# Performance work log

Measured on AMD Instinct MI355X. Metric: run time of the kernel, lower is better.

## Reference

```python
import jax, jax.numpy as jnp
import numpy as np

B, L, D, H, V = 4, 2048, 512, 8, 50257
NCAND, K, MAXM, NL, DFF = 64, 5, 10, 2, 4 * 512
HD = D // H


def _ln(x, g, b, eps=1e-5):
    m = jnp.mean(x, -1, keepdims=True)
    v = jnp.mean((x - m) ** 2, -1, keepdims=True)
    return (x - m) * jax.lax.rsqrt(v + eps) * g + b


def _mha(x, in_w, in_b, out_w, out_b):
    Bx, Lx, Dx = x.shape
    qkv = x @ in_w.T + in_b                      # [B,L,3D]
    q, k, v = jnp.split(qkv, 3, axis=-1)
    heads = lambda t: t.reshape(Bx, Lx, H, HD).transpose(0, 2, 1, 3)  # [B,H,L,hd]
    q, k, v = heads(q), heads(k), heads(v)
    s = jnp.einsum('bhqd,bhkd->bhqk', q, k) * np.float32(1.0 / np.sqrt(HD))
    a = jax.nn.softmax(s, axis=-1)
    o = jnp.einsum('bhqk,bhkd->bhqd', a, v).transpose(0, 2, 1, 3).reshape(Bx, Lx, Dx)
    return o @ out_w.T + out_b


def _encoder(x, p):
    # torch TransformerEncoderLayer default: post-LN, ReLU, dropout off (eval)
    for i in range(NL):
        x = _ln(x + _mha(x, p['attn_in_w'][i], p['attn_in_b'][i], p['attn_out_w'][i], p['attn_out_b'][i]), p['ln1_g'][i], p['ln1_b'][i])
        h = jax.nn.relu(x @ p['ffn_w1'][i].T + p['ffn_b1'][i]) @ p['ffn_w2'][i].T + p['ffn_b2'][i]
        x = _ln(x + h, p['ln2_g'][i], p['ln2_b'][i])
    return x


def _forward(token_ids, candidate_embeds, p):
    x = p['tok_emb'][token_ids] + p['pos_emb'][jnp.arange(L)][None]
    hidden = _encoder(x, p)                                  # [B,L,D]
    start_logits = hidden @ p['start_w'] + p['start_b']      # [B,L]
    end_logits = hidden @ p['end_w'] + p['end_b']
    s_idx = jax.lax.top_k(start_logits, K)[1]                # [B,K]
    e_idx = jax.lax.top_k(end_logits, K)[1]
    valid = (e_idx >= s_idx) & ((e_idx - s_idx) < MAXM)      # span validity mask
    h_s = jnp.take_along_axis(hidden, s_idx[..., None], axis=1)  # [B,K,D]
    h_e = jnp.take_along_axis(hidden, e_idx[..., None], axis=1)
    feat = jnp.concatenate([h_s, h_e, h_s * h_e], axis=-1)   # [B,K,3D]
    span = jax.nn.relu(feat @ p['span_w1'].T + p['span_b1']) @ p['span_w2'].T + p['span_b2']
    # compact valid spans to the front (ragged-to-padded), pad rest with zeros
    order = jnp.argsort((~valid).astype(jnp.int32), axis=1)  # stable: valid first
    span = jnp.take_along_axis(span, order[..., None], axis=1)
    vs = jnp.take_along_axis(valid, order, axis=1)
    span = span * vs[..., None].astype(span.dtype)           # [B,K,D]
    mp = span @ p['mention_w'].T + p['mention_b']
    cp = candidate_embeds @ p['entity_w'].T + p['entity_b']
    scores = jnp.einsum('bmd,bmcd->bmc', mp, cp)             # [B,K,NCAND]
    return span, start_logits, end_logits, hidden, scores


PARAM_KEYS = ['tok_emb', 'pos_emb', 'attn_in_w', 'attn_in_b', 'attn_out_w', 'attn_out_b',
              'ln1_g', 'ln1_b', 'ffn_w1', 'ffn_b1', 'ffn_w2', 'ffn_b2', 'ln2_g', 'ln2_b',
              'start_w', 'start_b', 'end_w', 'end_b', 'span_w1', 'span_b1', 'span_w2', 'span_b2',
              'mention_w', 'mention_b', 'entity_w', 'entity_b']


def setup_inputs() -> dict:
    key = jax.random.key(0)
    ks = iter(jax.random.split(key, 32))
    n = lambda shape, s=0.02: jax.random.normal(next(ks), shape, jnp.float32) * s
    return {
        'token_ids': jax.random.randint(next(ks), (B, L), 0, V),
        'candidate_embeds': jax.random.normal(next(ks), (B, K, NCAND, D), jnp.float32),
        'tok_emb': n((V, D)), 'pos_emb': n((L, D)),
        'attn_in_w': n((NL, 3 * D, D)), 'attn_in_b': n((NL, 3 * D)),
        'attn_out_w': n((NL, D, D)), 'attn_out_b': n((NL, D)),
        'ln1_g': jnp.ones((NL, D)), 'ln1_b': jnp.zeros((NL, D)),
        'ffn_w1': n((NL, DFF, D)), 'ffn_b1': n((NL, DFF)),
        'ffn_w2': n((NL, D, DFF)), 'ffn_b2': n((NL, D)),
        'ln2_g': jnp.ones((NL, D)), 'ln2_b': jnp.zeros((NL, D)),
        'start_w': n((D,)), 'start_b': jnp.zeros(()),
        'end_w': n((D,)), 'end_b': jnp.zeros(()),
        'span_w1': n((D, 3 * D)), 'span_b1': jnp.zeros((D,)),
        'span_w2': n((D, D)), 'span_b2': jnp.zeros((D,)),
        'mention_w': n((D, D)), 'mention_b': jnp.zeros((D,)),
        'entity_w': n((D, D)), 'entity_b': jnp.zeros((D,)),
    }


def reference(token_ids, candidate_embeds, tok_emb, pos_emb, attn_in_w, attn_in_b, attn_out_w, attn_out_b,
              ln1_g, ln1_b, ffn_w1, ffn_b1, ffn_w2, ffn_b2, ln2_g, ln2_b,
              start_w, start_b, end_w, end_b, span_w1, span_b1, span_w2, span_b2,
              mention_w, mention_b, entity_w, entity_b):
    loc = locals()
    p = {k: loc[k] for k in PARAM_KEYS}
    return _forward(token_ids, candidate_embeds, p)
```

## Files before the change

### kernel.cpp

```cpp
#include <hip/hip_runtime.h>
#include <hip/hip_bf16.h>
#include <cstddef>

#define BQ 4
#define LQ 2048
#define DQ 512
#define HQ 8
#define HDQ 64
#define KQ 5
#define MAXMQ 10

typedef __attribute__((ext_vector_type(8))) __bf16 bf16x8;
typedef __attribute__((ext_vector_type(4))) float f32x4;

__device__ inline void gload_lds16(const void* g, void* l) {
  __builtin_amdgcn_global_load_lds(
      (const __attribute__((address_space(1))) unsigned*)g,
      (__attribute__((address_space(3))) unsigned*)l, 16, 0, 0);
}

__device__ inline unsigned pack_bf16(float a, float b) {
  unsigned short ua = __builtin_bit_cast(unsigned short, (__bf16)a);
  unsigned short ub = __builtin_bit_cast(unsigned short, (__bf16)b);
  return (unsigned)ua | ((unsigned)ub << 16);
}

__device__ inline unsigned pack2(__bf16 a, __bf16 b) {
  return (unsigned)__builtin_bit_cast(unsigned short, a) |
         ((unsigned)__builtin_bit_cast(unsigned short, b) << 16);
}

__global__ __launch_bounds__(256) void cvt4_kernel(
    const float* __restrict__ s0, const float* __restrict__ s1,
    const float* __restrict__ s2, const float* __restrict__ s3,
    __bf16* __restrict__ d0, __bf16* __restrict__ d1,
    __bf16* __restrict__ d2, __bf16* __restrict__ d3) {
  size_t g = ((size_t)blockIdx.x * 256 + threadIdx.x) * 8;
  const float* src; __bf16* dst; size_t e;
  if (g < 1572864)      { src = s0; dst = d0; e = g; }
  else if (g < 2097152) { src = s1; dst = d1; e = g - 1572864; }
  else if (g < 4194304) { src = s2; dst = d2; e = g - 2097152; }
  else                  { src = s3; dst = d3; e = g - 4194304; }
  float4 a = *(const float4*)(src + e);
  float4 b = *(const float4*)(src + e + 4);
  bf16x8 t;
  t[0] = (__bf16)a.x; t[1] = (__bf16)a.y; t[2] = (__bf16)a.z; t[3] = (__bf16)a.w;
  t[4] = (__bf16)b.x; t[5] = (__bf16)b.y; t[6] = (__bf16)b.z; t[7] = (__bf16)b.w;
  *(bf16x8*)(dst + e) = t;
}

__global__ __launch_bounds__(256) void transpose512_kernel(const float* __restrict__ in,
                                                           float* __restrict__ out) {
  __shared__ float t[32][33];
  int bx = blockIdx.x & 15, by = blockIdx.x >> 4;
  int cx = threadIdx.x & 31, ry = threadIdx.x >> 5;
  #pragma unroll
  for (int i = 0; i < 4; ++i)
    t[ry + i * 8][cx] = in[(size_t)(by * 32 + ry + i * 8) * 512 + bx * 32 + cx];
  __syncthreads();
  #pragma unroll
  for (int i = 0; i < 4; ++i)
    out[(size_t)(bx * 32 + ry + i * 8) * 512 + by * 32 + cx] = t[cx][ry + i * 8];
}

__global__ __launch_bounds__(256) void embed_kernel(const int* __restrict__ tok,
    const float* __restrict__ te, const float* __restrict__ pe,
    float* __restrict__ x, __bf16* __restrict__ xb) {
  int row = blockIdx.x;
  int l = row & (LQ - 1);
  int t = tok[row];
  const float* trow = te + (size_t)t * DQ;
  const float* prow = pe + (size_t)l * DQ;
  float* xr = x + (size_t)row * DQ;
  __bf16* xbr = xb + (size_t)row * DQ;
  for (int d = threadIdx.x; d < DQ; d += 256) {
    float v = trow[d] + prow[d];
    xr[d] = v;
    xbr[d] = (__bf16)v;
  }
}

template<int BN, bool RELU, bool HASRES, bool WF32, bool WBF16>
__global__ __launch_bounds__(256) void bgemm_kernel(
    const __bf16* __restrict__ A, const __bf16* __restrict__ W,
    const float* __restrict__ bias, const float* __restrict__ R,
    float* __restrict__ C, __bf16* __restrict__ Cb, int M, int N, int K) {
  __shared__ __bf16 As[2][128][32];
  __shared__ __bf16 Bs[2][BN][32];
  constexpr int NF = BN / 32;
  const int tid = threadIdx.x;
  const int w = tid >> 6, lane = tid & 63;
  const int lr = lane & 15, lg = lane >> 4;
  const int wr = w >> 1, wc = w & 1;
  const int m0 = blockIdx.y * 128, n0 = blockIdx.x * BN;

  f32x4 acc[4][NF];
  #pragma unroll
  for (int m = 0; m < 4; ++m)
    #pragma unroll
    for (int n = 0; n < NF; ++n) acc[m][n] = f32x4{0.f, 0.f, 0.f, 0.f};

  const int srowA = w * 32 + (lane >> 2);
  const int scol = (lane & 3) * 8;
  const int srowB = (BN == 128) ? srowA : (w * 16 + (lane >> 2));
  const __bf16* Ag = A + (size_t)(m0 + srowA) * K + scol;
  const __bf16* Bg = W + (size_t)(n0 + srowB) * K + scol;

  gload_lds16(Ag, &As[0][w * 32][0]);
  gload_lds16(Ag + 16 * K, &As[0][w * 32 + 16][0]);
  if (BN == 128) {
    gload_lds16(Bg, &Bs[0][(w * 32) % BN][0]);
    gload_lds16(Bg + 16 * K, &Bs[0][(w * 32 + 16) % BN][0]);
  } else {
    gload_lds16(Bg, &Bs[0][(w * 16) % BN][0]);
  }

  const int NT = K / 32;
  for (int t = 0; t < NT; ++t) {
    const int cur = t & 1;
    __syncthreads();
    if (t + 1 < NT) {
      const int k1 = (t + 1) * 32;
      gload_lds16(Ag + k1, &As[cur ^ 1][w * 32][0]);
      gload_lds16(Ag + 16 * K + k1, &As[cur ^ 1][w * 32 + 16][0]);
      if (BN == 128) {
        gload_lds16(Bg + k1, &Bs[cur ^ 1][(w * 32) % BN][0]);
        gload_lds16(Bg + 16 * K + k1, &Bs[cur ^ 1][(w * 32 + 16) % BN][0]);
      } else {
        gload_lds16(Bg + k1, &Bs[cur ^ 1][(w * 16) % BN][0]);
      }
    }
    bf16x8 af[4], bfr[NF];
    #pragma unroll
    for (int m = 0; m < 4; ++m) af[m] = *(bf16x8*)&As[cur][wr * 64 + m * 16 + lr][lg * 8];
    #pragma unroll
    for (int n = 0; n < NF; ++n) bfr[n] = *(bf16x8*)&Bs[cur][wc * (BN / 2) + n * 16 + lr][lg * 8];
    #pragma unroll
    for (int m = 0; m < 4; ++m)
      #pragma unroll
      for (int n = 0; n < NF; ++n)
        acc[m][n] = __builtin_amdgcn_mfma_f32_16x16x32_bf16(af[m], bfr[n], acc[m][n], 0, 0, 0);
  }

  const int crow = m0 + wr * 64 + lg * 4;
  const int ccol = n0 + wc * (BN / 2) + lr;
  #pragma unroll
  for (int n = 0; n < NF; ++n) {
    int gc = ccol + n * 16;
    float bn = bias ? bias[gc] : 0.f;
    #pragma unroll
    for (int m = 0; m < 4; ++m) {
      #pragma unroll
      for (int reg = 0; reg < 4; ++reg) {
        int gr = crow + m * 16 + reg;
        float v = acc[m][n][reg] + bn;
        if (HASRES) v += R[(size_t)gr * N + gc];
        if (RELU) v = fmaxf(v, 0.f);
        if (WF32) C[(size_t)gr * N + gc] = v;
        if (WBF16) Cb[(size_t)gr * N + gc] = (__bf16)v;
      }
    }
  }
}

template<int MR, bool RELU, bool MASK>
__global__ __launch_bounds__(256) void tinygemm_kernel(
    const float* __restrict__ A, const float* __restrict__ W,
    const float* __restrict__ bias, const int* __restrict__ vs,
    float* __restrict__ C, int N, int K) {
  int n = blockIdx.x * 4 + (threadIdx.x >> 6);
  int lane = threadIdx.x & 63;
  if (n >= N) return;
  const float* wr = W + (size_t)n * K;
  float acc[MR];
  #pragma unroll
  for (int m = 0; m < MR; ++m) acc[m] = 0.f;
  for (int k = lane; k < K; k += 64) {
    float wv = wr[k];
    #pragma unroll
    for (int m = 0; m < MR; ++m)
      acc[m] += A[(size_t)m * K + k] * wv;
  }
  #pragma unroll
  for (int m = 0; m < MR; ++m) {
    #pragma unroll
    for (int off = 32; off; off >>= 1) acc[m] += __shfl_xor(acc[m], off);
  }
  if (lane == 0) {
    float bn = bias ? bias[n] : 0.f;
    #pragma unroll
    for (int m = 0; m < MR; ++m) {
      float v = acc[m] + bn;
      if (RELU) v = fmaxf(v, 0.f);
      if (MASK) v *= (float)vs[m];
      C[(size_t)m * N + n] = v;
    }
  }
}

__global__ __launch_bounds__(512) void attn_mfma_kernel(const __bf16* __restrict__ qkv,
                                                        __bf16* __restrict__ ob) {
  __shared__ __bf16 Ks[2][4096];
  __shared__ __bf16 Vt[2][64][72];
  __shared__ __bf16 Ps[8][1024];

  const int tid = threadIdx.x;
  const int wave = tid >> 6;
  const int lane = tid & 63;
  const int lr = lane & 15;
  const int lg = lane >> 4;

  const int bid = blockIdx.x;
  const int swz = (bid & 7) * 64 + (bid >> 3);
  const int bh = swz >> 4;
  const int qb = swz & 15;
  const int b = bh >> 3, h = bh & 7;
  const int q0 = qb * 128 + wave * 16;

  const __bf16* base = qkv + (size_t)b * LQ * 1536;

  bf16x8 aq[2];
  {
    const __bf16* qp = base + (size_t)(q0 + lr) * 1536 + h * 64 + lg * 8;
    aq[0] = *(const bf16x8*)qp;
    aq[1] = *(const bf16x8*)(qp + 32);
  }

  const int krow = tid >> 3;
  const int kdc = (tid & 7) ^ (krow & 7);
  const __bf16* gK = base + (size_t)krow * 1536 + 512 + h * 64 + kdc * 8;

  const int pr = tid >> 3, vdc = tid & 7;
  const bool vth = tid < 256;
  const __bf16* gV = base + (size_t)(2 * pr) * 1536 + 1024 + h * 64 + vdc * 8;
  const int pc2 = 2 * (pr & 3) + 8 * ((pr >> 2) ^ vdc);

  const int STEP = 64 * 1536;

  float mx = -1e30f, lsum = 0.f;
  f32x4 o_acc[4];
  #pragma unroll
  for (int df = 0; df < 4; ++df) o_acc[df] = f32x4{0.f, 0.f, 0.f, 0.f};

  const float KE = 0.125f * 1.44269504f;

  gload_lds16(gK, &Ks[0][64 * wave * 8]);
  if (vth) {
    bf16x8 v0 = *(const bf16x8*)gV;
    bf16x8 v1 = *(const bf16x8*)(gV + 1536);
    #pragma unroll
    for (int i = 0; i < 8; ++i)
      *(unsigned*)&Vt[0][vdc * 8 + i][pc2] = pack2(v0[i], v1[i]);
  }
  gK += STEP; gV += STEP;

  for (int kt = 0; kt < LQ / 64; ++kt) {
    const int cur = kt & 1;
    __syncthreads();
    bf16x8 nv0, nv1;
    const bool more = kt < LQ / 64 - 1;
    if (more) {
      gload_lds16(gK, &Ks[cur ^ 1][64 * wave * 8]);
      if (vth) {
        nv0 = *(const bf16x8*)gV;
        nv1 = *(const bf16x8*)(gV + 1536);
      }
      gK += STEP; gV += STEP;
    }

    f32x4 s[4];
    #pragma unroll
    for (int f = 0; f < 4; ++f) {
      f32x4 acc = f32x4{0.f, 0.f, 0.f, 0.f};
      #pragma unroll
      for (int c = 0; c < 2; ++c) {
        bf16x8 ak = *(bf16x8*)&Ks[cur][(f * 16 + lr) * 64 + (((4 * c + lg) ^ (lr & 7)) << 3)];
        acc = __builtin_amdgcn_mfma_f32_16x16x32_bf16(ak, aq[c], acc, 0, 0, 0);
      }
      s[f] = acc;
    }

    float rm = fmaxf(fmaxf(fmaxf(s[0][0], s[0][1]), fmaxf(s[0][2], s[0][3])),
                     fmaxf(fmaxf(s[1][0], s[1][1]), fmaxf(s[1][2], s[1][3])));
    rm = fmaxf(rm, fmaxf(fmaxf(fmaxf(s[2][0], s[2][1]), fmaxf(s[2][2], s[2][3])),
                         fmaxf(fmaxf(s[3][0], s[3][1]), fmaxf(s[3][2], s[3][3]))));
    rm = fmaxf(rm, __shfl_xor(rm, 16));
    rm = fmaxf(rm, __shfl_xor(rm, 32));
    if (!__all((rm - mx) * KE <= 8.f)) {
      float nm = fmaxf(mx, rm);
      float cor = exp2f((mx - nm) * KE);
      mx = nm;
      lsum *= cor;
      #pragma unroll
      for (int df = 0; df < 4; ++df) o_acc[df] *= cor;
    }
    float rs = 0.f;
    #pragma unroll
    for (int f = 0; f < 4; ++f)
      #pragma unroll
      for (int r = 0; r < 4; ++r) {
        float p = exp2f((s[f][r] - mx) * KE);
        s[f][r] = p;
        rs += p;
      }
    rs += __shfl_xor(rs, 16);
    rs += __shfl_xor(rs, 32);
    lsum += rs;

    #pragma unroll
    for (int f = 0; f < 4; ++f) {
      uint2 pv;
      pv.x = pack_bf16(s[f][0], s[f][1]);
      pv.y = pack_bf16(s[f][2], s[f][3]);
      int chunk = 2 * f + (lg >> 1);
      int eoff = ((chunk ^ (lr & 7)) << 3) + ((lg & 1) << 2);
      *(uint2*)&Ps[wave][lr * 64 + eoff] = pv;
    }

    #pragma unroll
    for (int kc = 0; kc < 2; ++kc) {
      bf16x8 bp = *(bf16x8*)&Ps[wave][lr * 64 + (((4 * kc + lg) ^ (lr & 7)) << 3)];
      #pragma unroll
      for (int df = 0; df < 4; ++df) {
        int vrow = df * 16 + lr;
        int pb = (((4 * kc + lg) ^ ((vrow >> 3) & 7)) << 3);
        bf16x8 av = *(bf16x8*)&Vt[cur][vrow][pb];
        o_acc[df] = __builtin_amdgcn_mfma_f32_16x16x32_bf16(av, bp, o_acc[df], 0, 0, 0);
      }
    }

    if (more && vth) {
      #pragma unroll
      for (int i = 0; i < 8; ++i)
        *(unsigned*)&Vt[cur ^ 1][vdc * 8 + i][pc2] = pack2(nv0[i], nv1[i]);
    }
  }

  float inv = 1.f / lsum;
  __bf16* orow = ob + ((size_t)(b * LQ) + q0 + lr) * DQ + h * 64 + lg * 4;
  #pragma unroll
  for (int df = 0; df < 4; ++df) {
    uint2 ov;
    ov.x = pack_bf16(o_acc[df][0] * inv, o_acc[df][1] * inv);
    ov.y = pack_bf16(o_acc[df][2] * inv, o_acc[df][3] * inv);
    *(uint2*)(orow + df * 16) = ov;
  }
}

__global__ __launch_bounds__(256) void ln_kernel(const float* __restrict__ t,
    const float* __restrict__ g, const float* __restrict__ bb,
    float* __restrict__ xo, __bf16* __restrict__ xb) {
  int row = blockIdx.x;
  const float* tr = t + (size_t)row * DQ;
  int tid = threadIdx.x;
  float v0 = tr[tid], v1 = tr[tid + 256];
  float s = v0 + v1, ss = v0 * v0 + v1 * v1;
  #pragma unroll
  for (int off = 32; off; off >>= 1) { s += __shfl_xor(s, off); ss += __shfl_xor(ss, off); }
  __shared__ float rs[4], rss[4];
  int w = tid >> 6;
  if ((tid & 63) == 0) { rs[w] = s; rss[w] = ss; }
  __syncthreads();
  s = rs[0] + rs[1] + rs[2] + rs[3];
  ss = rss[0] + rss[1] + rss[2] + rss[3];
  float mean = s * (1.f / 512.f);
  float var = ss * (1.f / 512.f) - mean * mean;
  float r = rsqrtf(var + 1e-5f);
  float* xr = xo + (size_t)row * DQ;
  __bf16* xbr = xb + (size_t)row * DQ;
  float o0 = (v0 - mean) * r * g[tid] + bb[tid];
  float o1 = (v1 - mean) * r * g[tid + 256] + bb[tid + 256];
  xr[tid] = o0; xr[tid + 256] = o1;
  xbr[tid] = (__bf16)o0; xbr[tid + 256] = (__bf16)o1;
}

__global__ __launch_bounds__(256) void logits_kernel(const float* __restrict__ hidden,
    const float* __restrict__ sw, const float* __restrict__ sb,
    const float* __restrict__ ew, const float* __restrict__ eb,
    float* __restrict__ osl, float* __restrict__ oel) {
  int row = blockIdx.x * 4 + (threadIdx.x >> 6);
  int lane = threadIdx.x & 63;
  const float* hr = hidden + (size_t)row * DQ;
  float a = 0.f, b2 = 0.f;
  #pragma unroll
  for (int i = 0; i < 8; ++i) {
    int d = lane + i * 64;
    float h = hr[d];
    a += h * sw[d];
    b2 += h * ew[d];
  }
  #pragma unroll
  for (int off = 32; off; off >>= 1) { a += __shfl_xor(a, off); b2 += __shfl_xor(b2, off); }
  if (lane == 0) { osl[row] = a + sb[0]; oel[row] = b2 + eb[0]; }
}

__global__ void topk_kernel(const float* __restrict__ slog, const float* __restrict__ elog,
                            int* __restrict__ sidx, int* __restrict__ eidx) {
  int b = blockIdx.x & 3;
  int which = blockIdx.x >> 2;
  const float* lg = (which ? elog : slog) + (size_t)b * LQ;
  int* outp = (which ? eidx : sidx) + b * KQ;
  int lane = threadIdx.x;
  int ch[KQ];
  for (int k = 0; k < KQ; ++k) {
    float bv = -1e38f; int bi = 1 << 30;
    for (int i = lane; i < LQ; i += 64) {
      bool skip = false;
      for (int t = 0; t < k; ++t) if (ch[t] == i) skip = true;
      float v = lg[i];
      if (!skip && (v > bv || (v == bv && i < bi))) { bv = v; bi = i; }
    }
    #pragma unroll
    for (int off = 32; off; off >>= 1) {
      float ov = __shfl_xor(bv, off); int oi = __shfl_xor(bi, off);
      if (ov > bv || (ov == bv && oi < bi)) { bv = ov; bi = oi; }
    }
    ch[k] = bi;
    if (lane == 0) outp[k] = bi;
  }
}

__global__ void vo_kernel(const int* __restrict__ sidx, const int* __restrict__ eidx,
                          int* __restrict__ order, int* __restrict__ vs) {
  int b = threadIdx.x;
  if (b >= BQ) return;
  int val[KQ];
  for (int k = 0; k < KQ; ++k) {
    int s = sidx[b * KQ + k], e = eidx[b * KQ + k];
    val[k] = (e >= s && (e - s) < MAXMQ) ? 1 : 0;
  }
  int j = 0;
  for (int k = 0; k < KQ; ++k) if (val[k])  { order[b * KQ + j] = k; vs[b * KQ + j] = 1; ++j; }
  for (int k = 0; k < KQ; ++k) if (!val[k]) { order[b * KQ + j] = k; vs[b * KQ + j] = 0; ++j; }
}

__global__ __launch_bounds__(256) void feat_kernel(const float* __restrict__ hidden,
    const int* __restrict__ sidx, const int* __restrict__ eidx,
    const int* __restrict__ order, float* __restrict__ feat) {
  int row = blockIdx.x;
  int b = row / KQ;
  int k = order[row];
  int si = sidx[b * KQ + k], ei = eidx[b * KQ + k];
  const float* hs = hidden + ((size_t)(b * LQ + si)) * DQ;
  const float* he = hidden + ((size_t)(b * LQ + ei)) * DQ;
  float* fr = feat + (size_t)row * (3 * DQ);
  for (int d = threadIdx.x; d < DQ; d += 256) {
    float a = hs[d], c = he[d];
    fr[d] = a; fr[DQ + d] = c; fr[2 * DQ + d] = a * c;
  }
}

__global__ __launch_bounds__(256) void scores_kernel(const float* __restrict__ cand,
    const float* __restrict__ mp, const float* __restrict__ u, const float* __restrict__ ebias,
    float* __restrict__ oscores) {
  int gw = blockIdx.x * 4 + (threadIdx.x >> 6);
  int lane = threadIdx.x & 63;
  int bj = gw >> 6;
  const float* ce = cand + (size_t)gw * DQ;
  const float* ur = u + (size_t)bj * DQ;
  const float* mr = mp + (size_t)bj * DQ;
  float s = 0.f;
  #pragma unroll
  for (int i = 0; i < 8; ++i) {
    int e = lane + i * 64;
    s += ce[e] * ur[e] + mr[e] * ebias[e];
  }
  #pragma unroll
  for (int off = 32; off; off >>= 1) s += __shfl_xor(s, off);
  if (lane == 0) oscores[gw] = s;
}

extern "C" void kernel_launch(void* const* d_in, const int* in_sizes, int n_in,
                              void* d_out, int out_size, void* d_ws, size_t ws_size,
                              hipStream_t stream) {
  const int*   token_ids = (const int*)d_in[0];
  const float* cand    = (const float*)d_in[1];
  const float* tok_emb = (const float*)d_in[2];
  const float* pos_emb = (const float*)d_in[3];
  const float* ain_w   = (const float*)d_in[4];
  const float* ain_b   = (const float*)d_in[5];
  const float* aout_w  = (const float*)d_in[6];
  const float* aout_b  = (const float*)d_in[7];
  const float* ln1g    = (const float*)d_in[8];
  const float* ln1b    = (const float*)d_in[9];
  const float* fw1     = (const float*)d_in[10];
  const float* fb1     = (const float*)d_in[11];
  const float* fw2     = (const float*)d_in[12];
  const float* fb2     = (const float*)d_in[13];
  const float* ln2g    = (const float*)d_in[14];
  const float* ln2b    = (const float*)d_in[15];
  const float* sw      = (const float*)d_in[16];
  const float* sb      = (const float*)d_in[17];
  const float* ew      = (const float*)d_in[18];
  const float* eb      = (const float*)d_in[19];
  const float* sp_w1   = (const float*)d_in[20];
  const float* sp_b1   = (const float*)d_in[21];
  const float* sp_w2   = (const float*)d_in[22];
  const float* sp_b2   = (const float*)d_in[23];
  const float* m_w     = (const float*)d_in[24];
  const float* m_b     = (const float*)d_in[25];
  const float* e_w     = (const float*)d_in[26];
  const float* e_b     = (const float*)d_in[27];

  const int M = BQ * LQ;
  float* out = (float*)d_out;
  float* out_span   = out;
  float* out_sl     = out + 10240;
  float* out_el     = out + 18432;
  float* out_hidden = out + 26624;
  float* out_scores = out + 4220928;

  float* ws  = (float*)d_ws;
  float* X    = ws;
  float* T    = ws + 4194304;
  __bf16* BIGb = (__bf16*)(ws + 8388608);
  __bf16* Xb   = (__bf16*)(ws + 16777216);
  __bf16* Ob   = (__bf16*)(ws + 18874368);
  __bf16* ain_wb  = (__bf16*)(ws + 20971520);
  __bf16* aout_wb = (__bf16*)(ws + 21757952);
  __bf16* fw1b    = (__bf16*)(ws + 22020096);
  __bf16* fw2b    = (__bf16*)(ws + 23068672);
  float* e_wT     = ws + 24117248;
  int*   SIDX  = (int*)(ws + 29360128);
  int*   EIDX  = SIDX + 20;
  int*   ORDER = EIDX + 20;
  int*   VS    = ORDER + 20;
  float* FEAT    = ws + 29360208;
  float* SPANH   = FEAT + 20 * 1536;
  float* MP      = SPANH + 10240;
  float* U       = MP + 10240;

  cvt4_kernel<<<3072, 256, 0, stream>>>(ain_w, aout_w, fw1, fw2,
                                        ain_wb, aout_wb, fw1b, fw2b);
  transpose512_kernel<<<256, 256, 0, stream>>>(e_w, e_wT);

  embed_kernel<<<M, 256, 0, stream>>>(token_ids, tok_emb, pos_emb, X, Xb);

  for (int l = 0; l < 2; ++l) {
    float* Xout = (l == 1) ? out_hidden : X;
    bgemm_kernel<128, false, false, false, true><<<dim3(12, 64), 256, 0, stream>>>(
        Xb, ain_wb + (size_t)l * 1536 * 512, ain_b + l * 1536, nullptr,
        nullptr, BIGb, M, 1536, 512);
    attn_mfma_kernel<<<512, 512, 0, stream>>>(BIGb, Ob);
    bgemm_kernel<64, false, true, true, false><<<dim3(8, 64), 256, 0, stream>>>(
        Ob, aout_wb + (size_t)l * 512 * 512, aout_b + l * 512, X,
        T, nullptr, M, 512, 512);
    ln_kernel<<<M, 256, 0, stream>>>(T, ln1g + l * 512, ln1b + l * 512, X, Xb);
    bgemm_kernel<128, true, false, false, true><<<dim3(16, 64), 256, 0, stream>>>(
        Xb, fw1b + (size_t)l * 2048 * 512, fb1 + l * 2048, nullptr,
        nullptr, BIGb, M, 2048, 512);
    bgemm_kernel<64, false, true, true, false><<<dim3(8, 64), 256, 0, stream>>>(
        BIGb, fw2b + (size_t)l * 512 * 2048, fb2 + l * 512, X,
        T, nullptr, M, 512, 2048);
    ln_kernel<<<M, 256, 0, stream>>>(T, ln2g + l * 512, ln2b + l * 512, Xout, Xb);
  }

  logits_kernel<<<M / 4, 256, 0, stream>>>(out_hidden, sw, sb, ew, eb, out_sl, out_el);
  topk_kernel<<<8, 64, 0, stream>>>(out_sl, out_el, SIDX, EIDX);
  vo_kernel<<<1, 64, 0, stream>>>(SIDX, EIDX, ORDER, VS);
  feat_kernel<<<20, 256, 0, stream>>>(out_hidden, SIDX, EIDX, ORDER, FEAT);
  tinygemm_kernel<20, true, false><<<128, 256, 0, stream>>>(
      FEAT, sp_w1, sp_b1, nullptr, SPANH, 512, 1536);
  tinygemm_kernel<20, false, true><<<128, 256, 0, stream>>>(
      SPANH, sp_w2, sp_b2, VS, out_span, 512, 512);
  tinygemm_kernel<20, false, false><<<128, 256, 0, stream>>>(
      out_span, m_w, m_b, nullptr, MP, 512, 512);
  tinygemm_kernel<20, false, false><<<128, 256, 0, stream>>>(
      MP, e_wT, nullptr, nullptr, U, 512, 512);
  scores_kernel<<<320, 256, 0, stream>>>(cand, MP, U, e_b, out_scores);
}
```

Measured before the change: 511.8 us.

## Keep residual stream in bf16, drop fp32 activations, add setprio and unroll

The residual stream and the pre-LayerNorm buffers move from fp32 to bf16 across embed, the GEMM epilogues and LayerNorm. This halves residual read and write traffic, and fp32 hidden is now written only for the final layer output. The GEMM and attention inner loops are manually unrolled by two with constant buffer indices, and s_setprio is raised around the MFMA blocks. The risk is extra rounding error, because residual sums are now rounded to bf16 at each layer.

```diff
diff --git a/kernel.cpp b/kernel.cpp
--- a/kernel.cpp
+++ b/kernel.cpp
@@ -28,6 +28,13 @@
 __device__ inline unsigned pack2(__bf16 a, __bf16 b) {
   return (unsigned)__builtin_bit_cast(unsigned short, a) |
          ((unsigned)__builtin_bit_cast(unsigned short, b) << 16);
+}
+
+__device__ inline float bf_lo(unsigned u) {
+  return (float)__builtin_bit_cast(__bf16, (unsigned short)(u & 0xffff));
+}
+__device__ inline float bf_hi(unsigned u) {
+  return (float)__builtin_bit_cast(__bf16, (unsigned short)(u >> 16));
 }
 
 __global__ __launch_bounds__(256) void cvt4_kernel(
@@ -65,26 +72,21 @@
 
 __global__ __launch_bounds__(256) void embed_kernel(const int* __restrict__ tok,
     const float* __restrict__ te, const float* __restrict__ pe,
-    float* __restrict__ x, __bf16* __restrict__ xb) {
+    __bf16* __restrict__ xb) {
   int row = blockIdx.x;
   int l = row & (LQ - 1);
   int t = tok[row];
-  const float* trow = te + (size_t)t * DQ;
-  const float* prow = pe + (size_t)l * DQ;
-  float* xr = x + (size_t)row * DQ;
-  __bf16* xbr = xb + (size_t)row * DQ;
-  for (int d = threadIdx.x; d < DQ; d += 256) {
-    float v = trow[d] + prow[d];
-    xr[d] = v;
-    xbr[d] = (__bf16)v;
-  }
-}
-
-template<int BN, bool RELU, bool HASRES, bool WF32, bool WBF16>
+  int d = 2 * threadIdx.x;
+  float2 tv = *(const float2*)&te[(size_t)t * DQ + d];
+  float2 pv = *(const float2*)&pe[(size_t)l * DQ + d];
+  *(unsigned*)&xb[(size_t)row * DQ + d] = pack_bf16(tv.x + pv.x, tv.y + pv.y);
+}
+
+template<int BN, bool RELU, bool HASRES>
 __global__ __launch_bounds__(256) void bgemm_kernel(
     const __bf16* __restrict__ A, const __bf16* __restrict__ W,
-    const float* __restrict__ bias, const float* __restrict__ R,
-    float* __restrict__ C, __bf16* __restrict__ Cb, int M, int N, int K) {
+    const float* __restrict__ bias, const __bf16* __restrict__ R,
+    __bf16* __restrict__ Cb, int M, int N, int K) {
   __shared__ __bf16 As[2][128][32];
   __shared__ __bf16 Bs[2][BN][32];
   constexpr int NF = BN / 32;
@@ -106,41 +108,39 @@
   const __bf16* Ag = A + (size_t)(m0 + srowA) * K + scol;
   const __bf16* Bg = W + (size_t)(n0 + srowB) * K + scol;
 
-  gload_lds16(Ag, &As[0][w * 32][0]);
-  gload_lds16(Ag + 16 * K, &As[0][w * 32 + 16][0]);
-  if (BN == 128) {
-    gload_lds16(Bg, &Bs[0][(w * 32) % BN][0]);
-    gload_lds16(Bg + 16 * K, &Bs[0][(w * 32 + 16) % BN][0]);
-  } else {
-    gload_lds16(Bg, &Bs[0][(w * 16) % BN][0]);
-  }
-
   const int NT = K / 32;
-  for (int t = 0; t < NT; ++t) {
-    const int cur = t & 1;
+
+  auto stage = [&](int t, int buf) {
+    const int k1 = t * 32;
+    gload_lds16(Ag + k1, &As[buf][w * 32][0]);
+    gload_lds16(Ag + 16 * K + k1, &As[buf][w * 32 + 16][0]);
+    if (BN == 128) {
+      gload_lds16(Bg + k1, &Bs[buf][(w * 32) % BN][0]);
+      gload_lds16(Bg + 16 * K + k1, &Bs[buf][(w * 32 + 16) % BN][0]);
+    } else {
+      gload_lds16(Bg + k1, &Bs[buf][(w * 16) % BN][0]);
+    }
+  };
+
+  auto step = [&](int t, int cur) {
     __syncthreads();
-    if (t + 1 < NT) {
-      const int k1 = (t + 1) * 32;
-      gload_lds16(Ag + k1, &As[cur ^ 1][w * 32][0]);
-      gload_lds16(Ag + 16 * K + k1, &As[cur ^ 1][w * 32 + 16][0]);
-      if (BN == 128) {
-        gload_lds16(Bg + k1, &Bs[cur ^ 1][(w * 32) % BN][0]);
-        gload_lds16(Bg + 16 * K + k1, &Bs[cur ^ 1][(w * 32 + 16) % BN][0]);
-      } else {
-        gload_lds16(Bg + k1, &Bs[cur ^ 1][(w * 16) % BN][0]);
-      }
-    }
+    if (t + 1 < NT) stage(t + 1, cur ^ 1);
     bf16x8 af[4], bfr[NF];
     #pragma unroll
     for (int m = 0; m < 4; ++m) af[m] = *(bf16x8*)&As[cur][wr * 64 + m * 16 + lr][lg * 8];
     #pragma unroll
     for (int n = 0; n < NF; ++n) bfr[n] = *(bf16x8*)&Bs[cur][wc * (BN / 2) + n * 16 + lr][lg * 8];
+    __builtin_amdgcn_s_setprio(1);
     #pragma unroll
     for (int m = 0; m < 4; ++m)
       #pragma unroll
       for (int n = 0; n < NF; ++n)
         acc[m][n] = __builtin_amdgcn_mfma_f32_16x16x32_bf16(af[m], bfr[n], acc[m][n], 0, 0, 0);
-  }
+    __builtin_amdgcn_s_setprio(0);
+  };
+
+  stage(0, 0);
+  for (int t = 0; t < NT; t += 2) { step(t, 0); step(t + 1, 1); }
 
   const int crow = m0 + wr * 64 + lg * 4;
   const int ccol = n0 + wc * (BN / 2) + lr;
@@ -154,10 +154,9 @@
       for (int reg = 0; reg < 4; ++reg) {
         int gr = crow + m * 16 + reg;
         float v = acc[m][n][reg] + bn;
-        if (HASRES) v += R[(size_t)gr * N + gc];
+        if (HASRES) v += (float)R[(size_t)gr * N + gc];
         if (RELU) v = fmaxf(v, 0.f);
-        if (WF32) C[(size_t)gr * N + gc] = v;
-        if (WBF16) Cb[(size_t)gr * N + gc] = (__bf16)v;
+        Cb[(size_t)gr * N + gc] = (__bf16)v;
       }
     }
   }
@@ -254,11 +253,9 @@
   }
   gK += STEP; gV += STEP;
 
-  for (int kt = 0; kt < LQ / 64; ++kt) {
-    const int cur = kt & 1;
+  auto tile = [&](int cur, bool more) {
     __syncthreads();
     bf16x8 nv0, nv1;
-    const bool more = kt < LQ / 64 - 1;
     if (more) {
       gload_lds16(gK, &Ks[cur ^ 1][64 * wave * 8]);
       if (vth) {
@@ -269,6 +266,7 @@
     }
 
     f32x4 s[4];
+    __builtin_amdgcn_s_setprio(1);
     #pragma unroll
     for (int f = 0; f < 4; ++f) {
       f32x4 acc = f32x4{0.f, 0.f, 0.f, 0.f};
@@ -279,6 +277,7 @@
       }
       s[f] = acc;
     }
+    __builtin_amdgcn_s_setprio(0);
 
     float rm = fmaxf(fmaxf(fmaxf(s[0][0], s[0][1]), fmaxf(s[0][2], s[0][3])),
                      fmaxf(fmaxf(s[1][0], s[1][1]), fmaxf(s[1][2], s[1][3])));
@@ -320,6 +319,7 @@
     #pragma unroll
     for (int kc = 0; kc < 2; ++kc) {
       bf16x8 bp = *(bf16x8*)&Ps[wave][lr * 64 + (((4 * kc + lg) ^ (lr & 7)) << 3)];
+      __builtin_amdgcn_s_setprio(1);
       #pragma unroll
       for (int df = 0; df < 4; ++df) {
         int vrow = df * 16 + lr;
@@ -327,6 +327,7 @@
         bf16x8 av = *(bf16x8*)&Vt[cur][vrow][pb];
         o_acc[df] = __builtin_amdgcn_mfma_f32_16x16x32_bf16(av, bp, o_acc[df], 0, 0, 0);
       }
+      __builtin_amdgcn_s_setprio(0);
     }
 
     if (more && vth) {
@@ -334,6 +335,11 @@
       for (int i = 0; i < 8; ++i)
         *(unsigned*)&Vt[cur ^ 1][vdc * 8 + i][pc2] = pack2(nv0[i], nv1[i]);
     }
+  };
+
+  for (int kt = 0; kt < LQ / 64; kt += 2) {
+    tile(0, true);
+    tile(1, kt + 1 != LQ / 64 - 1);
   }
 
   float inv = 1.f / lsum;
@@ -347,13 +353,14 @@
   }
 }
 
-__global__ __launch_bounds__(256) void ln_kernel(const float* __restrict__ t,
+template<bool WF32>
+__global__ __launch_bounds__(256) void ln_kernel(const __bf16* __restrict__ t,
     const float* __restrict__ g, const float* __restrict__ bb,
-    float* __restrict__ xo, __bf16* __restrict__ xb) {
+    __bf16* __restrict__ xb, float* __restrict__ xf) {
   int row = blockIdx.x;
-  const float* tr = t + (size_t)row * DQ;
   int tid = threadIdx.x;
-  float v0 = tr[tid], v1 = tr[tid + 256];
+  unsigned u = *(const unsigned*)&t[(size_t)row * DQ + 2 * tid];
+  float v0 = bf_lo(u), v1 = bf_hi(u);
   float s = v0 + v1, ss = v0 * v0 + v1 * v1;
   #pragma unroll
   for (int off = 32; off; off >>= 1) { s += __shfl_xor(s, off); ss += __shfl_xor(ss, off); }
@@ -366,12 +373,15 @@
   float mean = s * (1.f / 512.f);
   float var = ss * (1.f / 512.f) - mean * mean;
   float r = rsqrtf(var + 1e-5f);
-  float* xr = xo + (size_t)row * DQ;
-  __bf16* xbr = xb + (size_t)row * DQ;
-  float o0 = (v0 - mean) * r * g[tid] + bb[tid];
-  float o1 = (v1 - mean) * r * g[tid + 256] + bb[tid + 256];
-  xr[tid] = o0; xr[tid + 256] = o1;
-  xbr[tid] = (__bf16)o0; xbr[tid + 256] = (__bf16)o1;
+  float2 gg = *(const float2*)&g[2 * tid];
+  float2 bv = *(const float2*)&bb[2 * tid];
+  float o0 = (v0 - mean) * r * gg.x + bv.x;
+  float o1 = (v1 - mean) * r * gg.y + bv.y;
+  *(unsigned*)&xb[(size_t)row * DQ + 2 * tid] = pack_bf16(o0, o1);
+  if (WF32) {
+    float2 of; of.x = o0; of.y = o1;
+    *(float2*)&xf[(size_t)row * DQ + 2 * tid] = of;
+  }
 }
 
 __global__ __launch_bounds__(256) void logits_kernel(const float* __restrict__ hidden,
@@ -511,22 +521,21 @@
   float* out_scores = out + 4220928;
 
   float* ws  = (float*)d_ws;
-  float* X    = ws;
-  float* T    = ws + 4194304;
-  __bf16* BIGb = (__bf16*)(ws + 8388608);
-  __bf16* Xb   = (__bf16*)(ws + 16777216);
-  __bf16* Ob   = (__bf16*)(ws + 18874368);
-  __bf16* ain_wb  = (__bf16*)(ws + 20971520);
-  __bf16* aout_wb = (__bf16*)(ws + 21757952);
-  __bf16* fw1b    = (__bf16*)(ws + 22020096);
-  __bf16* fw2b    = (__bf16*)(ws + 23068672);
-  float* e_wT     = ws + 24117248;
-  int*   SIDX  = (int*)(ws + 29360128);
+  __bf16* BIGb = (__bf16*)ws;
+  __bf16* Xb   = (__bf16*)(ws + 8388608);
+  __bf16* Ob   = (__bf16*)(ws + 10485760);
+  __bf16* Tb   = (__bf16*)(ws + 12582912);
+  __bf16* ain_wb  = (__bf16*)(ws + 14680064);
+  __bf16* aout_wb = (__bf16*)(ws + 15466496);
+  __bf16* fw1b    = (__bf16*)(ws + 15728640);
+  __bf16* fw2b    = (__bf16*)(ws + 16777216);
+  float* e_wT     = ws + 17825792;
+  int*   SIDX  = (int*)(ws + 18088064);
   int*   EIDX  = SIDX + 20;
   int*   ORDER = EIDX + 20;
   int*   VS    = ORDER + 20;
-  float* FEAT    = ws + 29360208;
-  float* SPANH   = FEAT + 20 * 1536;
+  float* FEAT    = ws + 18088192;
+  float* SPANH   = FEAT + 30720;
   float* MP      = SPANH + 10240;
   float* U       = MP + 10240;
 
@@ -534,25 +543,29 @@
                                         ain_wb, aout_wb, fw1b, fw2b);
   transpose512_kernel<<<256, 256, 0, stream>>>(e_w, e_wT);
 
-  embed_kernel<<<M, 256, 0, stream>>>(token_ids, tok_emb, pos_emb, X, Xb);
+  embed_kernel<<<M, 256, 0, stream>>>(token_ids, tok_emb, pos_emb, Xb);
 
   for (int l = 0; l < 2; ++l) {
-    float* Xout = (l == 1) ? out_hidden : X;
-    bgemm_kernel<128, false, false, false, true><<<dim3(12, 64), 256, 0, stream>>>(
+    bgemm_kernel<128, false, false><<<dim3(12, 64), 256, 0, stream>>>(
         Xb, ain_wb + (size_t)l * 1536 * 512, ain_b + l * 1536, nullptr,
-        nullptr, BIGb, M, 1536, 512);
+        BIGb, M, 1536, 512);
     attn_mfma_kernel<<<512, 512, 0, stream>>>(BIGb, Ob);
-    bgemm_kernel<64, false, true, true, false><<<dim3(8, 64), 256, 0, stream>>>(
-        Ob, aout_wb + (size_t)l * 512 * 512, aout_b + l * 512, X,
-        T, nullptr, M, 512, 512);
-    ln_kernel<<<M, 256, 0, stream>>>(T, ln1g + l * 512, ln1b + l * 512, X, Xb);
-    bgemm_kernel<128, true, false, false, true><<<dim3(16, 64), 256, 0, stream>>>(
+    bgemm_kernel<64, false, true><<<dim3(8, 64), 256, 0, stream>>>(
+        Ob, aout_wb + (size_t)l * 512 * 512, aout_b + l * 512, Xb,
+        Tb, M, 512, 512);
+    ln_kernel<false><<<M, 256, 0, stream>>>(Tb, ln1g + l * 512, ln1b + l * 512,
+                                            Xb, nullptr);
+    bgemm_kernel<128, true, false><<<dim3(16, 64), 256, 0, stream>>>(
         Xb, fw1b + (size_t)l * 2048 * 512, fb1 + l * 2048, nullptr,
-        nullptr, BIGb, M, 2048, 512);
-    bgemm_kernel<64, false, true, true, false><<<dim3(8, 64), 256, 0, stream>>>(
-        BIGb, fw2b + (size_t)l * 512 * 2048, fb2 + l * 512, X,
-        T, nullptr, M, 512, 2048);
-    ln_kernel<<<M, 256, 0, stream>>>(T, ln2g + l * 512, ln2b + l * 512, Xout, Xb);
+        BIGb, M, 2048, 512);
+    bgemm_kernel<64, false, true><<<dim3(8, 64), 256, 0, stream>>>(
+        BIGb, fw2b + (size_t)l * 512 * 2048, fb2 + l * 512, Xb,
+        Tb, M, 512, 2048);
+    if (l == 0)
+      ln_kernel<false><<<M, 256, 0, stream>>>(Tb, ln2g, ln2b, Xb, nullptr);
+    else
+      ln_kernel<true><<<M, 256, 0, stream>>>(Tb, ln2g + 512, ln2b + 512,
+                                             Xb, out_hidden);
   }
 
   logits_kernel<<<M / 4, 256, 0, stream>>>(out_hidden, sw, sb, ew, eb, out_sl, out_el);
```

Result: no change. 505.7 us (-1.2%).
